# Kernel tuning notes

Measured on AMD Instinct MI355X. Metric: run time of the kernel, lower is better.

Reference implementation:

```python
import jax, jax.numpy as jnp
import numpy as np

N_NODES = 50000
N_EDGES = 800000
N_FEAT = 128
HIDDEN = 64
N_GRAPHS = 256


def setup_inputs() -> dict:
    key = jax.random.key(0)
    ks = jax.random.split(key, 10)
    x = jax.random.normal(ks[0], (N_NODES, N_FEAT), dtype=jnp.float32)
    edge_index = jax.random.randint(ks[1], (2, N_EDGES), 0, N_NODES, dtype=jnp.int64)
    batch = jnp.sort(jax.random.randint(ks[2], (N_NODES,), 0, N_GRAPHS, dtype=jnp.int64))
    s1 = 1.0 / np.sqrt(N_FEAT)
    s2 = 1.0 / np.sqrt(HIDDEN)
    W1 = jax.random.normal(ks[3], (N_FEAT, HIDDEN), dtype=jnp.float32) * s1
    b1 = jnp.zeros((HIDDEN,), dtype=jnp.float32)
    W2 = jax.random.normal(ks[4], (HIDDEN, HIDDEN), dtype=jnp.float32) * s2
    b2 = jnp.zeros((HIDDEN,), dtype=jnp.float32)
    Wm1 = jax.random.normal(ks[5], (HIDDEN, HIDDEN), dtype=jnp.float32) * s2
    bm1 = jnp.zeros((HIDDEN,), dtype=jnp.float32)
    Wm2 = jax.random.normal(ks[6], (HIDDEN, 1), dtype=jnp.float32) * s2
    bm2 = jnp.zeros((1,), dtype=jnp.float32)
    return {"x": x, "edge_index": edge_index, "batch": batch,
            "W1": W1, "b1": b1, "W2": W2, "b2": b2,
            "Wm1": Wm1, "bm1": bm1, "Wm2": Wm2, "bm2": bm2}


def _gcn_layer(h, W, b, src, dst, norm, n_nodes):
    # GCNConv: h @ W, then symmetric-normalized scatter-add over edges (+ self-loops), + bias
    h = h @ W
    msg = h[src] * norm[:, None]              # [E+N, H] gather + scale
    agg = jax.ops.segment_sum(msg, dst, num_segments=n_nodes)
    return agg + b


def reference(x, edge_index, batch, W1, b1, W2, b2, Wm1, bm1, Wm2, bm2):
    n = x.shape[0]
    loops = jnp.arange(n, dtype=edge_index.dtype)
    src = jnp.concatenate([edge_index[0], loops])  # self-loops as in PyG GCNConv
    dst = jnp.concatenate([edge_index[1], loops])
    deg = jax.ops.segment_sum(jnp.ones_like(dst, dtype=x.dtype), dst, num_segments=n)
    dis = jnp.where(deg > 0, jax.lax.rsqrt(deg), 0.0)  # deg^-1/2
    norm = dis[src] * dis[dst]

    h = jax.nn.relu(_gcn_layer(x, W1, b1, src, dst, norm, n))
    h = jax.nn.relu(_gcn_layer(h, W2, b2, src, dst, norm, n))

    # global mean pool over graphs
    sums = jax.ops.segment_sum(h, batch, num_segments=N_GRAPHS)
    cnts = jax.ops.segment_sum(jnp.ones((n,), dtype=h.dtype), batch, num_segments=N_GRAPHS)
    pooled = sums / jnp.maximum(cnts, 1.0)[:, None]

    # MLP head (dropout inactive at eval)
    out = jax.nn.relu(pooled @ Wm1 + bm1) @ Wm2 + bm2
    return out.reshape(-1)
```

## Files before the change

### kernel.cpp

```cpp
#include <hip/hip_runtime.h>

#define NN 50000
#define NE 800000
#define NF 128
#define NH 64
#define NG 256
#define NB 196
#define NC 196
#define CH 4096
#define CELL 80
#define CAP 5120

typedef __attribute__((ext_vector_type(8))) short bf16x8;
typedef __attribute__((ext_vector_type(4))) float f32x4;

static __device__ __forceinline__ float b2f(unsigned short u) {
    return __uint_as_float((unsigned)u << 16);
}
static __device__ __forceinline__ unsigned short f2bf(float f) {
    union { float f; unsigned u; } v; v.f = f;
    unsigned r = v.u + 0x7FFF + ((v.u >> 16) & 1);
    return (unsigned short)(r >> 16);
}
static __device__ __forceinline__ float lo16(unsigned u) {
    return __uint_as_float(u << 16);
}
static __device__ __forceinline__ float hi16(unsigned u) {
    return __uint_as_float(u & 0xFFFF0000u);
}

__global__ __launch_bounds__(256) void part_scatter(const int* __restrict__ ei,
                                                    int* __restrict__ histg,
                                                    int2* __restrict__ ebuf) {
    const int t = threadIdx.x;
    const int c = blockIdx.x;
    const int c0 = c * CH;
    __shared__ int hist[256];
    __shared__ int incl[256];
    __shared__ int lcur[256];
    __shared__ int2 lpairs[CH];

    hist[t] = 0;
    __syncthreads();

    int2 loc[16];
#pragma unroll
    for (int j = 0; j < 16; ++j) {
        int e = c0 + j * 256 + t;
        int s = -1, d = -1;
        if (e < NE) {
            s = ei[e]; d = ei[NE + e];
            atomicAdd(&hist[d >> 8], 1);
        }
        loc[j] = make_int2(s, d);
    }
    __syncthreads();

    int v = hist[t];
    incl[t] = v;
    __syncthreads();
    for (int off = 1; off < 256; off <<= 1) {
        int u = (t >= off) ? incl[t - off] : 0;
        __syncthreads();
        incl[t] += u;
        __syncthreads();
    }
    lcur[t] = incl[t] - v;
    if (t < NB) histg[c * NB + t] = v;
    __syncthreads();

#pragma unroll
    for (int j = 0; j < 16; ++j) {
        int d = loc[j].y;
        if (d >= 0) {
            int p = atomicAdd(&lcur[d >> 8], 1);
            lpairs[p] = loc[j];
        }
    }
    __syncthreads();

    const int total = incl[255];
    for (int p = t; p < total; p += 256) {
        int2 pr = lpairs[p];
        int b = pr.y >> 8;
        int i = p - (incl[b] - hist[b]);
        ebuf[(b * NC + c) * CELL + i] = pr;
    }
}

__global__ __launch_bounds__(256) void build_csr(const int2* __restrict__ ebuf,
                                                 const int* __restrict__ histg,
                                                 int2* __restrict__ row_range,
                                                 float* __restrict__ dis,
                                                 int* __restrict__ csr_src) {
    const int b = blockIdx.x, t = threadIdx.x;
    const int e0 = b * CAP;
    const int node = b * 256 + t;
    __shared__ int coff[256];
    __shared__ int deg_l[256];
    __shared__ int pre[256];
    __shared__ int cur[256];
    __shared__ int2 lpairs[CAP];
    __shared__ int lsrc[CAP];

    int cv = (t < NB) ? histg[t * NB + b] : 0;
    coff[t] = cv;
    __syncthreads();
    for (int off = 1; off < 256; off <<= 1) {
        int u = (t >= off) ? coff[t - off] : 0;
        __syncthreads();
        coff[t] += u;
        __syncthreads();
    }
    if (cv > 0) {
        const int2* src = &ebuf[(b * NC + t) * CELL];
        int dst = coff[t] - cv;
        for (int i = 0; i < cv; ++i)
            lpairs[dst + i] = src[i];
    }
    deg_l[t] = (node < NN) ? 1 : 0;
    __syncthreads();

    const int total = coff[255];
    for (int i = t; i < total; i += 256)
        atomicAdd(&deg_l[lpairs[i].y & 255], 1);
    __syncthreads();

    int v = deg_l[t];
    pre[t] = v;
    __syncthreads();
    for (int off = 1; off < 256; off <<= 1) {
        int u = (t >= off) ? pre[t - off] : 0;
        __syncthreads();
        pre[t] += u;
        __syncthreads();
    }
    int excl = pre[t] - v;
    cur[t] = 1;
    if (node < NN) {
        lsrc[excl] = node;
        row_range[node] = make_int2(e0 + excl, e0 + pre[t]);
        dis[node] = rsqrtf((float)v);
    }
    __syncthreads();
    for (int i = t; i < total; i += 256) {
        int2 p = lpairs[i];
        int d = p.y & 255;
        int pos = (pre[d] - deg_l[d]) + atomicAdd(&cur[d], 1);
        lsrc[pos] = p.x;
    }
    __syncthreads();
    const int tot_all = pre[255];
    for (int i = t; i < tot_all; i += 256)
        csr_src[e0 + i] = lsrc[i];
}

__global__ __launch_bounds__(256) void gemm1_mfma(const float* __restrict__ X,
                                                  const float* __restrict__ W,
                                                  const float* __restrict__ dis,
                                                  unsigned short* __restrict__ Y) {
    __shared__ unsigned short Xs[64 * 136];
    __shared__ unsigned int   Wt[64 * 68];
    const int t = threadIdx.x;
    const int base = blockIdx.x * 64;

    for (int i = t * 4; i < 64 * 128; i += 1024) {
        int node = i >> 7, k = i & 127;
        int gn = base + node; if (gn >= NN) gn = NN - 1;
        float4 v = *(const float4*)&X[(size_t)gn * 128 + k];
        ushort4 o = { f2bf(v.x), f2bf(v.y), f2bf(v.z), f2bf(v.w) };
        *(ushort4*)&Xs[node * 136 + k] = o;
    }
    for (int idx = t; idx < 64 * 64; idx += 256) {
        int n = idx & 63, kp = idx >> 6;
        float w0 = W[(2 * kp) * 64 + n];
        float w1 = W[(2 * kp + 1) * 64 + n];
        Wt[n * 68 + kp] = (unsigned)f2bf(w0) | ((unsigned)f2bf(w1) << 16);
    }
    __syncthreads();

    const int w = t >> 6;
    const int lane = t & 63;
    const int l15 = lane & 15;
    const int quad = lane >> 4;
    f32x4 acc[4] = {{0.f,0.f,0.f,0.f},{0.f,0.f,0.f,0.f},{0.f,0.f,0.f,0.f},{0.f,0.f,0.f,0.f}};
#pragma unroll
    for (int kk = 0; kk < 4; ++kk) {
        const bf16x8 a = *(const bf16x8*)&Xs[(w * 16 + l15) * 136 + quad * 8 + kk * 32];
#pragma unroll
        for (int nt = 0; nt < 4; ++nt) {
            const bf16x8 b = *(const bf16x8*)&Wt[(nt * 16 + l15) * 68 + quad * 4 + kk * 16];
            acc[nt] = __builtin_amdgcn_mfma_f32_16x16x32_bf16(a, b, acc[nt], 0, 0, 0);
        }
    }
    const int r0 = base + w * 16 + quad * 4;
    float4 d4 = *(const float4*)&dis[r0];
    const float dd[4] = { d4.x, d4.y, d4.z, d4.w };
#pragma unroll
    for (int reg = 0; reg < 4; ++reg) {
        const int row = r0 + reg;
        if (row < NN) {
#pragma unroll
            for (int nt = 0; nt < 4; ++nt)
                Y[(size_t)row * 64 + nt * 16 + l15] = f2bf(acc[nt][reg] * dd[reg]);
        }
    }
}

static __device__ __forceinline__ void acc8(float* acc, const uint4 u) {
    acc[0] += lo16(u.x); acc[1] += hi16(u.x);
    acc[2] += lo16(u.y); acc[3] += hi16(u.y);
    acc[4] += lo16(u.z); acc[5] += hi16(u.z);
    acc[6] += lo16(u.w); acc[7] += hi16(u.w);
}

static __device__ __forceinline__ void gather_rows(const unsigned short* __restrict__ h,
                                                   const int* __restrict__ csr_src,
                                                   int lo, int hi, int p8, float* acc) {
    int i = lo;
    for (; i + 2 <= hi; i += 2) {
        const int i0 = csr_src[i];
        const int i1 = csr_src[i + 1];
        const uint4 u0 = *(const uint4*)&h[(i0 << 6) + p8];
        const uint4 u1 = *(const uint4*)&h[(i1 << 6) + p8];
        acc8(acc, u0);
        acc8(acc, u1);
    }
    if (i < hi) {
        const int i0 = csr_src[i];
        acc8(acc, *(const uint4*)&h[(i0 << 6) + p8]);
    }
}

__global__ __launch_bounds__(256) void agg_gemv(const unsigned short* __restrict__ h,
                                                const int2* __restrict__ row_range,
                                                const int* __restrict__ csr_src,
                                                const float* __restrict__ dis,
                                                const float* __restrict__ b1,
                                                const float* __restrict__ W2,
                                                unsigned short* __restrict__ g) {
    __shared__ float W2s[64 * 64];
    __shared__ float aS[64 * 36];
    const int t = threadIdx.x;
    for (int i = t * 4; i < 4096; i += 1024)
        *(float4*)&W2s[i] = *(const float4*)&W2[i];

    const int base = blockIdx.x * 32;
    const int nloc = t >> 3;
    const int p8 = (t & 7) * 8;
    const int n = base + nloc;
    float acc[8] = {};
    if (n < NN) {
        const int2 rr = row_range[n];
        gather_rows(h, csr_src, rr.x, rr.y, p8, acc);
        const float dn = dis[n];
        const float4 bv0 = *(const float4*)&b1[p8];
        const float4 bv1 = *(const float4*)&b1[p8 + 4];
        acc[0] = fmaxf(acc[0] * dn + bv0.x, 0.f) * dn;
        acc[1] = fmaxf(acc[1] * dn + bv0.y, 0.f) * dn;
        acc[2] = fmaxf(acc[2] * dn + bv0.z, 0.f) * dn;
        acc[3] = fmaxf(acc[3] * dn + bv0.w, 0.f) * dn;
        acc[4] = fmaxf(acc[4] * dn + bv1.x, 0.f) * dn;
        acc[5] = fmaxf(acc[5] * dn + bv1.y, 0.f) * dn;
        acc[6] = fmaxf(acc[6] * dn + bv1.z, 0.f) * dn;
        acc[7] = fmaxf(acc[7] * dn + bv1.w, 0.f) * dn;
    }
#pragma unroll
    for (int j = 0; j < 8; ++j)
        aS[(p8 + j) * 36 + nloc] = acc[j];
    __syncthreads();

    const int n0 = (t & 7) * 4;
    const int c0 = (t >> 3) * 2;
    float a0x = 0, a0y = 0, a1x = 0, a1y = 0;
    float a2x = 0, a2y = 0, a3x = 0, a3y = 0;
#pragma unroll 8
    for (int k = 0; k < 64; ++k) {
        const float4 xv = *(const float4*)&aS[k * 36 + n0];
        const float2 wv = *(const float2*)&W2s[k * 64 + c0];
        a0x += xv.x * wv.x; a0y += xv.x * wv.y;
        a1x += xv.y * wv.x; a1y += xv.y * wv.y;
        a2x += xv.z * wv.x; a2y += xv.z * wv.y;
        a3x += xv.w * wv.x; a3y += xv.w * wv.y;
    }
    const int gn = base + n0;
    if (gn + 0 < NN) *(unsigned*)&g[(gn + 0) * 64 + c0] = (unsigned)f2bf(a0x) | ((unsigned)f2bf(a0y) << 16);
    if (gn + 1 < NN) *(unsigned*)&g[(gn + 1) * 64 + c0] = (unsigned)f2bf(a1x) | ((unsigned)f2bf(a1y) << 16);
    if (gn + 2 < NN) *(unsigned*)&g[(gn + 2) * 64 + c0] = (unsigned)f2bf(a2x) | ((unsigned)f2bf(a2y) << 16);
    if (gn + 3 < NN) *(unsigned*)&g[(gn + 3) * 64 + c0] = (unsigned)f2bf(a3x) | ((unsigned)f2bf(a3y) << 16);
}

__global__ __launch_bounds__(256) void agg_pool(const unsigned short* __restrict__ h,
                                                const int2* __restrict__ row_range,
                                                const int* __restrict__ csr_src,
                                                const float* __restrict__ dis,
                                                const float* __restrict__ bias,
                                                const int* __restrict__ batch,
                                                float* __restrict__ psum) {
    __shared__ float rowsL[32 * 68];
    __shared__ int nb[32];
    const int t = threadIdx.x;
    const int nloc = t >> 3;
    const int n = blockIdx.x * 32 + nloc;
    const int p8 = (t & 7) * 8;
    if ((t & 7) == 0) nb[nloc] = (n < NN) ? batch[n] : -1;
    if (n < NN) {
        const int2 rr = row_range[n];
        float acc[8] = {};
        gather_rows(h, csr_src, rr.x, rr.y, p8, acc);
        const float dn = dis[n];
        const float4 bv0 = *(const float4*)&bias[p8];
        const float4 bv1 = *(const float4*)&bias[p8 + 4];
        float4 r0, r1;
        r0.x = fmaxf(acc[0] * dn + bv0.x, 0.f);
        r0.y = fmaxf(acc[1] * dn + bv0.y, 0.f);
        r0.z = fmaxf(acc[2] * dn + bv0.z, 0.f);
        r0.w = fmaxf(acc[3] * dn + bv0.w, 0.f);
        r1.x = fmaxf(acc[4] * dn + bv1.x, 0.f);
        r1.y = fmaxf(acc[5] * dn + bv1.y, 0.f);
        r1.z = fmaxf(acc[6] * dn + bv1.z, 0.f);
        r1.w = fmaxf(acc[7] * dn + bv1.w, 0.f);
        *(float4*)&rowsL[nloc * 68 + p8] = r0;
        *(float4*)&rowsL[nloc * 68 + p8 + 4] = r1;
    }
    __syncthreads();
    if (t < 64) {
        float s = 0.f; int curg = -2;
        for (int r = 0; r < 32; ++r) {
            const int gg = nb[r];
            if (gg != curg) {
                if (curg >= 0) atomicAdd(&psum[curg * 64 + t], s);
                s = 0.f; curg = gg;
            }
            if (gg >= 0) s += rowsL[r * 68 + t];
        }
        if (curg >= 0) atomicAdd(&psum[curg * 64 + t], s);
    }
}

__global__ __launch_bounds__(64) void head_kernel(const float* __restrict__ psum,
                                                  const int* __restrict__ batch,
                                                  const float* __restrict__ Wm1,
                                                  const float* __restrict__ bm1,
                                                  const float* __restrict__ Wm2,
                                                  const float* __restrict__ bm2,
                                                  float* __restrict__ out) {
    const int g = blockIdx.x;
    const int t = threadIdx.x;
    int lo = 0, hi = NN;
    while (lo < hi) { int m = (lo + hi) >> 1; if (batch[m] < g) lo = m + 1; else hi = m; }
    const int s = lo;
    hi = NN;
    while (lo < hi) { int m = (lo + hi) >> 1; if (batch[m] < g + 1) lo = m + 1; else hi = m; }
    const int cnt = lo - s;

    __shared__ float pl[64];
    pl[t] = psum[g * 64 + t] / (float)(cnt > 0 ? cnt : 1);
    __syncthreads();
    float z = bm1[t];
#pragma unroll 8
    for (int k = 0; k < 64; ++k)
        z += pl[k] * Wm1[k * 64 + t];
    z = fmaxf(z, 0.f);
    float y = z * Wm2[t];
    for (int off = 32; off; off >>= 1) y += __shfl_down(y, off);
    if (t == 0) out[g] = y + bm2[0];
}

extern "C" void kernel_launch(void* const* d_in, const int* in_sizes, int n_in,
                              void* d_out, int out_size, void* d_ws, size_t ws_size,
                              hipStream_t stream) {
    const float* x   = (const float*)d_in[0];
    const int*   ei  = (const int*)d_in[1];
    const int*   bat = (const int*)d_in[2];
    const float* W1  = (const float*)d_in[3];
    const float* b1  = (const float*)d_in[4];
    const float* W2  = (const float*)d_in[5];
    const float* b2  = (const float*)d_in[6];
    const float* Wm1 = (const float*)d_in[7];
    const float* bm1 = (const float*)d_in[8];
    const float* Wm2 = (const float*)d_in[9];
    const float* bm2 = (const float*)d_in[10];
    float* out = (float*)d_out;

    char* w = (char*)d_ws;
    int*            histg     = (int*)           (w + 0);
    int2*           row_range = (int2*)          (w + 153664);
    float*          dis       = (float*)         (w + 553664);
    int*            csr_src   = (int*)           (w + 753664);
    int2*           ebuf      = (int2*)          (w + 4767744);
    unsigned short* bufA      = (unsigned short*)(w + 29353984);
    unsigned short* bufB      = (unsigned short*)(w + 35753984);
    float*          psum      = (float*)         (w + 42153984);

    hipMemsetAsync(psum, 0, NG * NH * sizeof(float), stream);
    part_scatter<<<NC, 256, 0, stream>>>(ei, histg, ebuf);
    build_csr   <<<NB, 256, 0, stream>>>(ebuf, histg, row_range, dis, csr_src);

    gemm1_mfma<<<(NN + 63) / 64, 256, 0, stream>>>(x, W1, dis, bufA);
    agg_gemv  <<<(NN + 31) / 32, 256, 0, stream>>>(bufA, row_range, csr_src, dis, b1, W2, bufB);
    agg_pool  <<<(NN + 31) / 32, 256, 0, stream>>>(bufB, row_range, csr_src, dis, b2, bat, psum);
    head_kernel<<<NG, 64, 0, stream>>>(psum, bat, Wm1, bm1, Wm2, bm2, out);
}
```

Before: 176.7 us.

## Use bf16 MFMA for layer-2 GEMV and unroll gather by four

The fused aggregate+GEMV kernel now packs the aggregated activations to bf16 in shared memory and runs the 32x64x64 product with bf16 MFMA instructions instead of scalar fp32 FMAs, with W2 converted and transposed into shared memory. The edge gather loop is also unrolled to four outstanding row loads per iteration to raise memory-level parallelism. The cost is an extra rounding of activations and weights to bf16 before the matmul, plus per-block conversion work for W2.

```diff
diff --git a/kernel.cpp b/kernel.cpp
--- a/kernel.cpp
+++ b/kernel.cpp
@@ -14,9 +14,6 @@
 typedef __attribute__((ext_vector_type(8))) short bf16x8;
 typedef __attribute__((ext_vector_type(4))) float f32x4;
 
-static __device__ __forceinline__ float b2f(unsigned short u) {
-    return __uint_as_float((unsigned)u << 16);
-}
 static __device__ __forceinline__ unsigned short f2bf(float f) {
     union { float f; unsigned u; } v; v.f = f;
     unsigned r = v.u + 0x7FFF + ((v.u >> 16) & 1);
@@ -218,13 +215,23 @@
                                                    const int* __restrict__ csr_src,
                                                    int lo, int hi, int p8, float* acc) {
     int i = lo;
+    for (; i + 4 <= hi; i += 4) {
+        const int i0 = csr_src[i];
+        const int i1 = csr_src[i + 1];
+        const int i2 = csr_src[i + 2];
+        const int i3 = csr_src[i + 3];
+        const uint4 u0 = *(const uint4*)&h[(i0 << 6) + p8];
+        const uint4 u1 = *(const uint4*)&h[(i1 << 6) + p8];
+        const uint4 u2 = *(const uint4*)&h[(i2 << 6) + p8];
+        const uint4 u3 = *(const uint4*)&h[(i3 << 6) + p8];
+        acc8(acc, u0); acc8(acc, u1); acc8(acc, u2); acc8(acc, u3);
+    }
     for (; i + 2 <= hi; i += 2) {
         const int i0 = csr_src[i];
         const int i1 = csr_src[i + 1];
         const uint4 u0 = *(const uint4*)&h[(i0 << 6) + p8];
         const uint4 u1 = *(const uint4*)&h[(i1 << 6) + p8];
-        acc8(acc, u0);
-        acc8(acc, u1);
+        acc8(acc, u0); acc8(acc, u1);
     }
     if (i < hi) {
         const int i0 = csr_src[i];
@@ -239,11 +246,15 @@
                                                 const float* __restrict__ b1,
                                                 const float* __restrict__ W2,
                                                 unsigned short* __restrict__ g) {
-    __shared__ float W2s[64 * 64];
-    __shared__ float aS[64 * 36];
+    __shared__ unsigned short W2b[64 * 72];
+    __shared__ unsigned short A[32 * 72];
     const int t = threadIdx.x;
-    for (int i = t * 4; i < 4096; i += 1024)
-        *(float4*)&W2s[i] = *(const float4*)&W2[i];
+    for (int idx = t; idx < 64 * 32; idx += 256) {
+        int n = idx & 63, kp = idx >> 6;
+        unsigned short w0 = f2bf(W2[(2 * kp) * 64 + n]);
+        unsigned short w1 = f2bf(W2[(2 * kp + 1) * 64 + n]);
+        *(unsigned*)&W2b[n * 72 + 2 * kp] = (unsigned)w0 | ((unsigned)w1 << 16);
+    }
 
     const int base = blockIdx.x * 32;
     const int nloc = t >> 3;
@@ -265,29 +276,40 @@
         acc[6] = fmaxf(acc[6] * dn + bv1.z, 0.f) * dn;
         acc[7] = fmaxf(acc[7] * dn + bv1.w, 0.f) * dn;
     }
-#pragma unroll
-    for (int j = 0; j < 8; ++j)
-        aS[(p8 + j) * 36 + nloc] = acc[j];
-    __syncthreads();
-
-    const int n0 = (t & 7) * 4;
-    const int c0 = (t >> 3) * 2;
-    float a0x = 0, a0y = 0, a1x = 0, a1y = 0;
-    float a2x = 0, a2y = 0, a3x = 0, a3y = 0;
-#pragma unroll 8
-    for (int k = 0; k < 64; ++k) {
-        const float4 xv = *(const float4*)&aS[k * 36 + n0];
-        const float2 wv = *(const float2*)&W2s[k * 64 + c0];
-        a0x += xv.x * wv.x; a0y += xv.x * wv.y;
-        a1x += xv.y * wv.x; a1y += xv.y * wv.y;
-        a2x += xv.z * wv.x; a2y += xv.z * wv.y;
-        a3x += xv.w * wv.x; a3y += xv.w * wv.y;
-    }
-    const int gn = base + n0;
-    if (gn + 0 < NN) *(unsigned*)&g[(gn + 0) * 64 + c0] = (unsigned)f2bf(a0x) | ((unsigned)f2bf(a0y) << 16);
-    if (gn + 1 < NN) *(unsigned*)&g[(gn + 1) * 64 + c0] = (unsigned)f2bf(a1x) | ((unsigned)f2bf(a1y) << 16);
-    if (gn + 2 < NN) *(unsigned*)&g[(gn + 2) * 64 + c0] = (unsigned)f2bf(a2x) | ((unsigned)f2bf(a2y) << 16);
-    if (gn + 3 < NN) *(unsigned*)&g[(gn + 3) * 64 + c0] = (unsigned)f2bf(a3x) | ((unsigned)f2bf(a3y) << 16);
+    uint4 pk;
+    pk.x = (unsigned)f2bf(acc[0]) | ((unsigned)f2bf(acc[1]) << 16);
+    pk.y = (unsigned)f2bf(acc[2]) | ((unsigned)f2bf(acc[3]) << 16);
+    pk.z = (unsigned)f2bf(acc[4]) | ((unsigned)f2bf(acc[5]) << 16);
+    pk.w = (unsigned)f2bf(acc[6]) | ((unsigned)f2bf(acc[7]) << 16);
+    *(uint4*)&A[nloc * 72 + p8] = pk;
+    __syncthreads();
+
+    const int w = t >> 6;
+    const int lane = t & 63;
+    const int l15 = lane & 15;
+    const int quad = lane >> 4;
+    const int mt = w & 1;
+    const int nq = (w >> 1) * 2;
+    const bf16x8 a0 = *(const bf16x8*)&A[(mt * 16 + l15) * 72 + quad * 8];
+    const bf16x8 a1 = *(const bf16x8*)&A[(mt * 16 + l15) * 72 + 32 + quad * 8];
+    const bf16x8 b00 = *(const bf16x8*)&W2b[(nq * 16 + l15) * 72 + quad * 8];
+    const bf16x8 b01 = *(const bf16x8*)&W2b[(nq * 16 + l15) * 72 + 32 + quad * 8];
+    const bf16x8 b10 = *(const bf16x8*)&W2b[((nq + 1) * 16 + l15) * 72 + quad * 8];
+    const bf16x8 b11 = *(const bf16x8*)&W2b[((nq + 1) * 16 + l15) * 72 + 32 + quad * 8];
+    f32x4 c0 = {0.f, 0.f, 0.f, 0.f}, c1 = {0.f, 0.f, 0.f, 0.f};
+    c0 = __builtin_amdgcn_mfma_f32_16x16x32_bf16(a0, b00, c0, 0, 0, 0);
+    c0 = __builtin_amdgcn_mfma_f32_16x16x32_bf16(a1, b01, c0, 0, 0, 0);
+    c1 = __builtin_amdgcn_mfma_f32_16x16x32_bf16(a0, b10, c1, 0, 0, 0);
+    c1 = __builtin_amdgcn_mfma_f32_16x16x32_bf16(a1, b11, c1, 0, 0, 0);
+    const int r0 = base + mt * 16 + quad * 4;
+#pragma unroll
+    for (int reg = 0; reg < 4; ++reg) {
+        const int row = r0 + reg;
+        if (row < NN) {
+            g[(size_t)row * 64 + nq * 16 + l15] = f2bf(c0[reg]);
+            g[(size_t)row * 64 + (nq + 1) * 16 + l15] = f2bf(c1[reg]);
+        }
+    }
 }
 
 __global__ __launch_bounds__(256) void agg_pool(const unsigned short* __restrict__ h,
```

Result: faster. 161.3 us (-8.7%).
